# Performance work log

Measured on AMD Instinct MI355X. Metric: run time of the kernel, lower is better.

## Reference

```python
import jax, jax.numpy as jnp
import numpy as np

N_NODES = 100000
N_EDGES = 1600000
D_FEAT = 64
NUM_HEADS = 4
HEAD_CH = 16
ALPHA = 0.2  # leaky_relu negative slope (Keras default)


def setup_inputs() -> dict:
    key = jax.random.key(0)
    ks = jax.random.split(key, 8)
    hc = NUM_HEADS * HEAD_CH
    scale = 1.0 / np.sqrt(D_FEAT)
    return {
        'node_features': jax.random.normal(ks[0], (N_NODES, D_FEAT), jnp.float32),
        'Wq': jax.random.normal(ks[1], (D_FEAT, hc), jnp.float32) * scale,
        'bq': jnp.zeros((hc,), jnp.float32),
        'Wv': jax.random.normal(ks[2], (D_FEAT, hc), jnp.float32) * scale,
        'bv': jnp.zeros((hc,), jnp.float32),
        'attn_kernel': jax.random.normal(ks[3], (HEAD_CH, NUM_HEADS), jnp.float32) / np.sqrt(HEAD_CH),
        'edge_source': jax.random.randint(ks[4], (N_EDGES,), 0, N_NODES, jnp.int32),
        'edge_target': jax.random.randint(ks[5], (N_EDGES,), 0, N_NODES, jnp.int32),
    }


def _gatv2(node_features, Wq, bq, Wv, bv, attn_kernel, edge_source, edge_target):
    # Dense transforms on nodes (small GEMMs), then reshape to heads.
    query = (node_features @ Wq + bq).reshape(N_NODES, NUM_HEADS, HEAD_CH)
    value = (node_features @ Wv + bv).reshape(N_NODES, NUM_HEADS, HEAD_CH)
    # Gather onto edges: receiver query, sender value.
    q_e = query[edge_target]           # [E, H, C]
    v_e = value[edge_source]           # [E, H, C]
    feat = jax.nn.leaky_relu(q_e + v_e, ALPHA)
    # EinsumDense '...ik,ki->...i' with kernel [C, H]
    logits = jnp.einsum('ehc,ch->eh', feat, attn_kernel)  # [E, H]
    # Segment softmax over receiver neighborhoods.
    seg_max = jax.ops.segment_max(logits, edge_target, num_segments=N_NODES)
    seg_max = jnp.where(jnp.isfinite(seg_max), seg_max, 0.0)
    exp = jnp.exp(logits - seg_max[edge_target])           # [E, H]
    denom = jax.ops.segment_sum(exp, edge_target, num_segments=N_NODES)
    denom = jnp.where(denom > 0, denom, 1.0)
    coef = exp / denom[edge_target]                        # [E, H]
    # Weighted scatter-sum of values to receivers.
    pooled = jax.ops.segment_sum(coef[:, :, None] * v_e, edge_target,
                                 num_segments=N_NODES)     # [N, H, C]
    out = pooled.reshape(N_NODES, NUM_HEADS * HEAD_CH)
    # NOTE: source code sets final activation to attention_activation (leaky_relu).
    return jax.nn.leaky_relu(out, ALPHA)


def reference(node_features, Wq, bq, Wv, bv, attn_kernel, edge_source, edge_target):
    return _gatv2(node_features, Wq, bq, Wv, bv, attn_kernel, edge_source, edge_target)
```

## Files before the change

kernel.cpp:

```cpp
#include <hip/hip_runtime.h>

#define NN 100000
#define NE 1600000
#define ALPHA 0.2f

#define BSH   9
#define NPBK  512
#define NBUCK ((NN + NPBK - 1) / NPBK)
#define NPB   256
#define CHUNK ((NE + NPB - 1) / NPB)

#define MTILES (NN / 16)
#define TBLKS  ((MTILES + 3) / 4)

typedef __attribute__((ext_vector_type(8))) short  short8;
typedef __attribute__((ext_vector_type(4))) float  f32x4;

__device__ __forceinline__ unsigned short f2bf(float f) {
    unsigned int u = __builtin_bit_cast(unsigned int, f);
    u += 0x7FFFu + ((u >> 16) & 1u);
    return (unsigned short)(u >> 16);
}
__device__ __forceinline__ float bf2fs(unsigned short u) {
    return __builtin_bit_cast(float, (unsigned int)u << 16);
}
__device__ __forceinline__ float bflo(unsigned int u) {
    return __builtin_bit_cast(float, u << 16);
}
__device__ __forceinline__ float bfhi(unsigned int u) {
    return __builtin_bit_cast(float, u & 0xFFFF0000u);
}

template<int CTRL>
__device__ __forceinline__ float dpp_add(float x) {
    int y = __builtin_amdgcn_update_dpp(0, __builtin_bit_cast(int, x),
                                        CTRL, 0xF, 0xF, true);
    return x + __builtin_bit_cast(float, y);
}

__device__ __forceinline__ int block_excl_scan_256(int val, int* lds4) {
    const int lane = threadIdx.x & 63;
    const int wid  = threadIdx.x >> 6;
    int incl = val;
    #pragma unroll
    for (int off = 1; off < 64; off <<= 1) {
        int t = __shfl_up(incl, off);
        if (lane >= off) incl += t;
    }
    if (lane == 63) lds4[wid] = incl;
    __syncthreads();
    int wbase = 0;
    #pragma unroll
    for (int w = 0; w < 4; w++) if (w < wid) wbase += lds4[w];
    __syncthreads();
    return wbase + incl - val;
}

__device__ __forceinline__ int block_excl_scan_512(int val, int* lds8) {
    const int lane = threadIdx.x & 63;
    const int wid  = threadIdx.x >> 6;
    int incl = val;
    #pragma unroll
    for (int off = 1; off < 64; off <<= 1) {
        int t = __shfl_up(incl, off);
        if (lane >= off) incl += t;
    }
    if (lane == 63) lds8[wid] = incl;
    __syncthreads();
    int wbase = 0;
    #pragma unroll
    for (int w = 0; w < 8; w++) if (w < wid) wbase += lds8[w];
    __syncthreads();
    return wbase + incl - val;
}

__global__ __launch_bounds__(256) void fused_tc_kernel(
    const float* __restrict__ nf, const float* __restrict__ Wq, const float* __restrict__ bq,
    const float* __restrict__ Wv, const float* __restrict__ bv,
    unsigned short* __restrict__ qbf, unsigned short* __restrict__ vbf,
    const int* __restrict__ etgt, int* __restrict__ hist, int* __restrict__ gtotal)
{
    __shared__ short8 sB[2][2][8][64];
    __shared__ float  sbias[128];
    __shared__ int    h[NBUCK];
    const int tid = threadIdx.x;

    if (blockIdx.x < NPB) {
        const int blk = blockIdx.x;
        for (int i = tid; i < NBUCK; i += 256) h[i] = 0;
        __syncthreads();
        const int e0 = blk * CHUNK;
        const int e1 = min(e0 + CHUNK, NE);
        for (int e = e0 + tid; e < e1; e += 256)
            atomicAdd(&h[etgt[e] >> BSH], 1);
        __syncthreads();
        for (int i = tid; i < NBUCK; i += 256) {
            int c = h[i];
            hist[blk * NBUCK + i] = c;
            if (c) atomicAdd(&gtotal[i], c);
        }
        return;
    }

    if (tid < 64)       sbias[tid] = bq[tid];
    else if (tid < 128) sbias[tid] = bv[tid - 64];

    for (int slot = tid; slot < 2 * 8 * 64; slot += 256) {
        const int lane  = slot & 63;
        const int ntile = (slot >> 6) & 7;
        const int kstep = slot >> 9;
        const int j     = ntile * 16 + (lane & 15);
        const int kbase = kstep * 32 + (lane >> 4) * 8;
        const float* W  = (j < 64) ? Wq : Wv;
        const int jj    = j & 63;
        short8 hi, lo;
        #pragma unroll
        for (int r = 0; r < 8; r++) {
            float w = W[(kbase + r) * 64 + jj];
            unsigned short hh = f2bf(w);
            lo[r] = (short)f2bf(w - bf2fs(hh));
            hi[r] = (short)hh;
        }
        sB[0][kstep][ntile][lane] = hi;
        sB[1][kstep][ntile][lane] = lo;
    }
    __syncthreads();

    const int lane  = tid & 63;
    const int wv_   = tid >> 6;
    const int row16 = lane & 15;
    const int kg    = lane >> 4;
    const int tb    = blockIdx.x - NPB;

    for (int wt = tb * 4 + wv_; wt < MTILES; wt += TBLKS * 4) {
        const int row = wt * 16 + row16;

        short8 ah[2], al[2];
        #pragma unroll
        for (int s = 0; s < 2; s++) {
            const float* ap = nf + (size_t)row * 64 + s * 32 + kg * 8;
            #pragma unroll
            for (int r = 0; r < 8; r++) {
                float x = ap[r];
                unsigned short hh = f2bf(x);
                al[s][r] = (short)f2bf(x - bf2fs(hh));
                ah[s][r] = (short)hh;
            }
        }

        #pragma unroll
        for (int nt = 0; nt < 8; nt++) {
            f32x4 acc = {0.f, 0.f, 0.f, 0.f};
            #pragma unroll
            for (int s = 0; s < 2; s++) {
                short8 bh = sB[0][s][nt][lane];
                short8 bl = sB[1][s][nt][lane];
                acc = __builtin_amdgcn_mfma_f32_16x16x32_bf16(ah[s], bh, acc, 0, 0, 0);
                acc = __builtin_amdgcn_mfma_f32_16x16x32_bf16(al[s], bh, acc, 0, 0, 0);
                acc = __builtin_amdgcn_mfma_f32_16x16x32_bf16(ah[s], bl, acc, 0, 0, 0);
            }
            const int col = nt * 16 + (lane & 15);
            const float b = sbias[col];
            unsigned short* outp = (col < 64) ? qbf : vbf;
            const int jj    = col & 63;
            const int rbase = wt * 16 + (lane >> 4) * 4;
            #pragma unroll
            for (int r = 0; r < 4; r++)
                outp[(size_t)(rbase + r) * 64 + jj] = f2bf(acc[r] + b);
        }
    }
}

__global__ __launch_bounds__(256) void colbase_kernel(
    const int* __restrict__ hist, const int* __restrict__ gtotal,
    int* __restrict__ bbase, int* __restrict__ colbase, int* __restrict__ offs)
{
    __shared__ int lds4[4];
    __shared__ int sb[256];
    const int bk = blockIdx.x;
    const int t  = threadIdx.x;

    int gval = (t < NBUCK) ? gtotal[t] : 0;
    int gex  = block_excl_scan_256(gval, lds4);
    sb[t] = gex;
    if (t == bk) bbase[bk] = gex;
    if (bk == 0 && t == NBUCK - 1) { bbase[NBUCK] = gex + gval; offs[NN] = NE; }
    __syncthreads();
    const int myBase = sb[bk];
    __syncthreads();

    int val = hist[t * NBUCK + bk];
    int ex  = block_excl_scan_256(val, lds4);
    colbase[t * NBUCK + bk] = myBase + ex;
}

__global__ __launch_bounds__(256) void partition_kernel(
    const int* __restrict__ esrc, const int* __restrict__ etgt,
    const int* __restrict__ colbase, unsigned int* __restrict__ packed)
{
    __shared__ int cur[NBUCK];
    const int blk = blockIdx.x;
    for (int i = threadIdx.x; i < NBUCK; i += 256)
        cur[i] = colbase[blk * NBUCK + i];
    __syncthreads();
    const int e0 = blk * CHUNK;
    const int e1 = min(e0 + CHUNK, NE);
    for (int e = e0 + threadIdx.x; e < e1; e += 256) {
        int t = etgt[e], s = esrc[e];
        int bk = t >> BSH;
        int pos = atomicAdd(&cur[bk], 1);
        packed[pos] = (unsigned)s | ((unsigned)(t & (NPBK - 1)) << 17);
    }
}

__global__ __launch_bounds__(512) void bucket_csr_kernel(
    const unsigned int* __restrict__ packed, const int* __restrict__ bbase,
    int* __restrict__ offs, int* __restrict__ ssrc)
{
    __shared__ int cnt[NPBK];
    __shared__ int lds8[8];
    const int bk  = blockIdx.x;
    const int tid = threadIdx.x;
    const int s0 = bbase[bk], s1 = bbase[bk + 1];
    cnt[tid] = 0;
    __syncthreads();
    for (int e = s0 + tid; e < s1; e += 512)
        atomicAdd(&cnt[packed[e] >> 17], 1);
    __syncthreads();
    int a  = cnt[tid];
    int ex = block_excl_scan_512(a, lds8);
    const int node = (bk << BSH) + tid;
    const int g = s0 + ex;
    if (node < NN) offs[node] = g;
    __syncthreads();
    cnt[tid] = g;
    __syncthreads();
    for (int e = s0 + tid; e < s1; e += 512) {
        unsigned p = packed[e];
        int pos = atomicAdd(&cnt[p >> 17], 1);
        ssrc[pos] = (int)(p & 0x1FFFFu);
    }
}

__device__ __forceinline__ uint4 ldraw16(const unsigned short* __restrict__ vb,
                                         int src, int s8) {
    return *(const uint4*)((const char*)vb + ((size_t)src << 7) + s8 * 16);
}

__global__ __launch_bounds__(256) void gather_kernel(
    const unsigned short* __restrict__ qb, const unsigned short* __restrict__ vb,
    const float* __restrict__ ak,
    const int* __restrict__ offs, const int* __restrict__ ssrc,
    float* __restrict__ out)
{
    const int node = (blockIdx.x * 256 + threadIdx.x) >> 6;
    const int lane = threadIdx.x & 63;
    if (node >= NN) return;
    const int eslot = lane >> 3;
    const int s8    = lane & 7;
    const int h     = s8 >> 1;

    const int start = offs[node];
    const int end   = offs[node + 1];

    if (start >= end) {
        if (lane < 8) {
            float4 z{0.f, 0.f, 0.f, 0.f};
            *(float4*)(out + (size_t)node * 64 + s8 * 8)     = z;
            *(float4*)(out + (size_t)node * 64 + s8 * 8 + 4) = z;
        }
        return;
    }
    const int end1 = end - 1;

    const float c6 = 0.6f * 1.44269504088896f;
    const float c4 = 0.4f * 1.44269504088896f;
    float a6[8], a4[8];
    #pragma unroll
    for (int j = 0; j < 8; j++) {
        float k = ak[((s8 & 1) * 8 + j) * 4 + h];
        a6[j] = c6 * k;  a4[j] = c4 * k;
    }

    const uint4 qraw = *(const uint4*)((const char*)qb + ((size_t)node << 7) + s8 * 16);
    float q[8];
    q[0] = bflo(qraw.x); q[1] = bfhi(qraw.x);
    q[2] = bflo(qraw.y); q[3] = bfhi(qraw.y);
    q[4] = bflo(qraw.z); q[5] = bfhi(qraw.z);
    q[6] = bflo(qraw.w); q[7] = bfhi(qraw.w);

    int i0 = ssrc[min(start +     eslot, end1)];
    int i1 = ssrc[min(start + 8 + eslot, end1)];
    uint4 rr0 = ldraw16(vb, i0, s8);
    uint4 rr1 = ldraw16(vb, i1, s8);
    int mi0 = ssrc[min(start + 16 + eslot, end1)];
    int mi1 = ssrc[min(start + 24 + eslot, end1)];

    float acc[8] = {0.f, 0.f, 0.f, 0.f, 0.f, 0.f, 0.f, 0.f};
    float ws = 0.f;

    for (int p = start; p < end; p += 16) {
        {
            float v[8];
            v[0] = bflo(rr0.x); v[1] = bfhi(rr0.x);
            v[2] = bflo(rr0.y); v[3] = bfhi(rr0.y);
            v[4] = bflo(rr0.z); v[5] = bfhi(rr0.z);
            v[6] = bflo(rr0.w); v[7] = bfhi(rr0.w);
            rr0 = ldraw16(vb, mi0, s8);
            mi0 = ssrc[min(p + 32 + eslot, end1)];
            float x = 0.f;
            #pragma unroll
            for (int j = 0; j < 8; j++) {
                float f = q[j] + v[j];
                x = fmaf(f, a6[j], x);
                x = fmaf(fabsf(f), a4[j], x);
            }
            x = dpp_add<0xB1>(x);
            float w = (p + eslot < end) ? __builtin_amdgcn_exp2f(x) : 0.f;
            ws += w;
            #pragma unroll
            for (int j = 0; j < 8; j++) acc[j] = fmaf(w, v[j], acc[j]);
        }
        {
            float v[8];
            v[0] = bflo(rr1.x); v[1] = bfhi(rr1.x);
            v[2] = bflo(rr1.y); v[3] = bfhi(rr1.y);
            v[4] = bflo(rr1.z); v[5] = bfhi(rr1.z);
            v[6] = bflo(rr1.w); v[7] = bfhi(rr1.w);
            rr1 = ldraw16(vb, mi1, s8);
            mi1 = ssrc[min(p + 40 + eslot, end1)];
            float x = 0.f;
            #pragma unroll
            for (int j = 0; j < 8; j++) {
                float f = q[j] + v[j];
                x = fmaf(f, a6[j], x);
                x = fmaf(fabsf(f), a4[j], x);
            }
            x = dpp_add<0xB1>(x);
            float w = (p + 8 + eslot < end) ? __builtin_amdgcn_exp2f(x) : 0.f;
            ws += w;
            #pragma unroll
            for (int j = 0; j < 8; j++) acc[j] = fmaf(w, v[j], acc[j]);
        }
    }

    #pragma unroll
    for (int m = 8; m <= 32; m <<= 1) {
        #pragma unroll
        for (int j = 0; j < 8; j++) acc[j] += __shfl_xor(acc[j], m);
        ws += __shfl_xor(ws, m);
    }

    if (lane < 8) {
        float inv = (ws > 0.f) ? __frcp_rn(ws) : 1.0f;
        float r[8];
        #pragma unroll
        for (int j = 0; j < 8; j++) {
            float t = acc[j] * inv;
            r[j] = fmaxf(t, ALPHA * t);
        }
        *(float4*)(out + (size_t)node * 64 + s8 * 8)     = float4{r[0], r[1], r[2], r[3]};
        *(float4*)(out + (size_t)node * 64 + s8 * 8 + 4) = float4{r[4], r[5], r[6], r[7]};
    }
}

extern "C" void kernel_launch(void* const* d_in, const int* in_sizes, int n_in,
                              void* d_out, int out_size, void* d_ws, size_t ws_size,
                              hipStream_t stream) {
    const float* nf   = (const float*)d_in[0];
    const float* Wq   = (const float*)d_in[1];
    const float* bq   = (const float*)d_in[2];
    const float* Wv   = (const float*)d_in[3];
    const float* bv   = (const float*)d_in[4];
    const float* ak   = (const float*)d_in[5];
    const int*   esrc = (const int*)d_in[6];
    const int*   etgt = (const int*)d_in[7];
    float* out = (float*)d_out;

    unsigned short* qbf     = (unsigned short*)d_ws;
    unsigned short* vbf     = qbf + (size_t)NN * 64;
    int*            offs    = (int*)(vbf + (size_t)NN * 64);
    int*            ssrc    = offs + (NN + 1);
    unsigned int*   packed  = (unsigned int*)(ssrc + NE);
    int*            hist    = (int*)(packed + NE);
    int*            colbase = hist + NPB * NBUCK;
    int*            gtotal  = colbase + NPB * NBUCK;
    int*            bbase   = gtotal + NBUCK;

    hipMemsetAsync(gtotal, 0, NBUCK * sizeof(int), stream);

    fused_tc_kernel<<<NPB + TBLKS, 256, 0, stream>>>(nf, Wq, bq, Wv, bv, qbf, vbf,
                                                     etgt, hist, gtotal);
    colbase_kernel<<<NBUCK, 256, 0, stream>>>(hist, gtotal, bbase, colbase, offs);
    partition_kernel<<<NPB, 256, 0, stream>>>(esrc, etgt, colbase, packed);
    bucket_csr_kernel<<<NBUCK, 512, 0, stream>>>(packed, bbase, offs, ssrc);
    gather_kernel<<<(NN * 64 + 255) / 256, 256, 0, stream>>>(qbf, vbf, ak, offs, ssrc, out);
}
```

Measured before the change: 119.6 us.

## Drop global atomic bucket totals and memset; trim split-bf16 GEMM to two MFMAs

Removes the hipMemsetAsync and the global atomicAdd of per-block bucket counts. Each colbase block now recomputes the bucket totals by summing the histogram columns itself. Separately, the node-feature operand is converted to a single bf16 value instead of a hi/lo pair, which cuts the projection GEMM from three MFMAs per k-step to two and drops the lo conversion work. The trade-off is lower precision in the q/v projections and redundant column summation in every colbase block.

New measurement: 113.1 us. -5.4%, faster.

```diff
diff --git a/kernel.cpp b/kernel.cpp
--- a/kernel.cpp
+++ b/kernel.cpp
@@ -78,7 +78,7 @@
     const float* __restrict__ nf, const float* __restrict__ Wq, const float* __restrict__ bq,
     const float* __restrict__ Wv, const float* __restrict__ bv,
     unsigned short* __restrict__ qbf, unsigned short* __restrict__ vbf,
-    const int* __restrict__ etgt, int* __restrict__ hist, int* __restrict__ gtotal)
+    const int* __restrict__ etgt, int* __restrict__ hist)
 {
     __shared__ short8 sB[2][2][8][64];
     __shared__ float  sbias[128];
@@ -94,11 +94,8 @@
         for (int e = e0 + tid; e < e1; e += 256)
             atomicAdd(&h[etgt[e] >> BSH], 1);
         __syncthreads();
-        for (int i = tid; i < NBUCK; i += 256) {
-            int c = h[i];
-            hist[blk * NBUCK + i] = c;
-            if (c) atomicAdd(&gtotal[i], c);
-        }
+        for (int i = tid; i < NBUCK; i += 256)
+            hist[blk * NBUCK + i] = h[i];
         return;
     }
 
@@ -135,17 +132,13 @@
     for (int wt = tb * 4 + wv_; wt < MTILES; wt += TBLKS * 4) {
         const int row = wt * 16 + row16;
 
-        short8 ah[2], al[2];
+        short8 ah[2];
         #pragma unroll
         for (int s = 0; s < 2; s++) {
             const float* ap = nf + (size_t)row * 64 + s * 32 + kg * 8;
             #pragma unroll
-            for (int r = 0; r < 8; r++) {
-                float x = ap[r];
-                unsigned short hh = f2bf(x);
-                al[s][r] = (short)f2bf(x - bf2fs(hh));
-                ah[s][r] = (short)hh;
-            }
+            for (int r = 0; r < 8; r++)
+                ah[s][r] = (short)f2bf(ap[r]);
         }
 
         #pragma unroll
@@ -153,11 +146,8 @@
             f32x4 acc = {0.f, 0.f, 0.f, 0.f};
             #pragma unroll
             for (int s = 0; s < 2; s++) {
-                short8 bh = sB[0][s][nt][lane];
-                short8 bl = sB[1][s][nt][lane];
-                acc = __builtin_amdgcn_mfma_f32_16x16x32_bf16(ah[s], bh, acc, 0, 0, 0);
-                acc = __builtin_amdgcn_mfma_f32_16x16x32_bf16(al[s], bh, acc, 0, 0, 0);
-                acc = __builtin_amdgcn_mfma_f32_16x16x32_bf16(ah[s], bl, acc, 0, 0, 0);
+                acc = __builtin_amdgcn_mfma_f32_16x16x32_bf16(ah[s], sB[0][s][nt][lane], acc, 0, 0, 0);
+                acc = __builtin_amdgcn_mfma_f32_16x16x32_bf16(ah[s], sB[1][s][nt][lane], acc, 0, 0, 0);
             }
             const int col = nt * 16 + (lane & 15);
             const float b = sbias[col];
@@ -172,7 +162,7 @@
 }
 
 __global__ __launch_bounds__(256) void colbase_kernel(
-    const int* __restrict__ hist, const int* __restrict__ gtotal,
+    const int* __restrict__ hist,
     int* __restrict__ bbase, int* __restrict__ colbase, int* __restrict__ offs)
 {
     __shared__ int lds4[4];
@@ -180,11 +170,15 @@
     const int bk = blockIdx.x;
     const int t  = threadIdx.x;
 
-    int gval = (t < NBUCK) ? gtotal[t] : 0;
-    int gex  = block_excl_scan_256(gval, lds4);
+    int csum = 0;
+    if (t < NBUCK) {
+        #pragma unroll 8
+        for (int b = 0; b < NPB; b++) csum += hist[b * NBUCK + t];
+    }
+    int gex = block_excl_scan_256(csum, lds4);
     sb[t] = gex;
     if (t == bk) bbase[bk] = gex;
-    if (bk == 0 && t == NBUCK - 1) { bbase[NBUCK] = gex + gval; offs[NN] = NE; }
+    if (bk == 0 && t == NBUCK - 1) { bbase[NBUCK] = gex + csum; offs[NN] = NE; }
     __syncthreads();
     const int myBase = sb[bk];
     __syncthreads();
@@ -384,14 +378,11 @@
     unsigned int*   packed  = (unsigned int*)(ssrc + NE);
     int*            hist    = (int*)(packed + NE);
     int*            colbase = hist + NPB * NBUCK;
-    int*            gtotal  = colbase + NPB * NBUCK;
-    int*            bbase   = gtotal + NBUCK;
-
-    hipMemsetAsync(gtotal, 0, NBUCK * sizeof(int), stream);
+    int*            bbase   = colbase + NPB * NBUCK;
 
     fused_tc_kernel<<<NPB + TBLKS, 256, 0, stream>>>(nf, Wq, bq, Wv, bv, qbf, vbf,
-                                                     etgt, hist, gtotal);
-    colbase_kernel<<<NBUCK, 256, 0, stream>>>(hist, gtotal, bbase, colbase, offs);
+                                                     etgt, hist);
+    colbase_kernel<<<NBUCK, 256, 0, stream>>>(hist, bbase, colbase, offs);
     partition_kernel<<<NPB, 256, 0, stream>>>(esrc, etgt, colbase, packed);
     bucket_csr_kernel<<<NBUCK, 512, 0, stream>>>(packed, bbase, offs, ssrc);
     gather_kernel<<<(NN * 64 + 255) / 256, 256, 0, stream>>>(qbf, vbf, ak, offs, ssrc, out);
```
